# Optimization experiments

Measured on AMD Instinct MI355X. Metric: run time of the kernel, lower is better.

Reference implementation:

```python
import jax, jax.numpy as jnp
import numpy as np
from functools import partial

B, T, H, W = 8, 256, 64, 64
D_MODEL, N_LAYERS, D_STATE = 256, 6, 16
D_INNER = 2 * D_MODEL
DT_RANK = 16  # ceil(256/16)
D_CONV = 4
CNN_Z = 32


def setup_inputs() -> dict:
    key = jax.random.key(0)
    ks = iter(jax.random.split(key, 64))
    r = lambda shape, s=0.02: jax.random.normal(next(ks), shape, dtype=jnp.float32) * s
    inp = {
        'x': jax.random.normal(next(ks), (B, T, 1, H, W), dtype=jnp.float32),
        # frozen CNN spatial encoder (1->16->32->32, stride-2 convs, global avg pool)
        'cnn_w1': r((16, 1, 3, 3)), 'cnn_b1': jnp.zeros((16,)),
        'cnn_w2': r((32, 16, 3, 3)), 'cnn_b2': jnp.zeros((32,)),
        'cnn_w3': r((32, 32, 3, 3)), 'cnn_b3': jnp.zeros((32,)),
        # fc_s2t: 32 -> 256
        'fc_w': r((D_MODEL, CNN_Z)), 'fc_b': jnp.zeros((D_MODEL,)),
        # Mamba, stacked over layers
        'norm_w': jnp.ones((N_LAYERS, D_MODEL)),
        'in_proj_w': r((N_LAYERS, 2 * D_INNER, D_MODEL)),
        'conv1d_w': r((N_LAYERS, D_INNER, D_CONV)),
        'conv1d_b': jnp.zeros((N_LAYERS, D_INNER)),
        'x_proj_w': r((N_LAYERS, DT_RANK + 2 * D_STATE, D_INNER)),
        'dt_proj_w': r((N_LAYERS, D_INNER, DT_RANK)),
        'dt_proj_b': jnp.full((N_LAYERS, D_INNER), -4.6),  # softplus ~ 0.01
        'A_log': jnp.tile(jnp.log(jnp.arange(1, D_STATE + 1, dtype=jnp.float32))[None, None, :], (N_LAYERS, D_INNER, 1)),
        'Dp': jnp.ones((N_LAYERS, D_INNER)),
        'out_proj_w': r((N_LAYERS, D_MODEL, D_INNER)),
        'norm_f_w': jnp.ones((D_MODEL,)),
        # prediction head: 256 -> 64 -> 1
        'head_w1': r((D_MODEL // 4, D_MODEL)), 'head_b1': jnp.zeros((D_MODEL // 4,)),
        'head_w2': r((1, D_MODEL // 4)), 'head_b2': jnp.zeros((1,)),
    }
    return inp


def _conv2d(x, w, b, stride):
    y = jax.lax.conv_general_dilated(x, w, (stride, stride), 'SAME',
                                     dimension_numbers=('NCHW', 'OIHW', 'NCHW'))
    return jax.nn.relu(y + b[None, :, None, None])


def _rmsnorm(x, w, eps=1e-5):
    return x * jax.lax.rsqrt(jnp.mean(x * x, axis=-1, keepdims=True) + eps) * w


def _selective_scan(u, delta, A, Bm, Cm, Dvec):
    # u,delta: (B,L,E); A: (E,N); Bm,Cm: (B,L,N); D: (E,)
    deltaA = jnp.exp(delta[..., None] * A)                       # (B,L,E,N)
    deltaBu = delta[..., None] * Bm[:, :, None, :] * u[..., None]  # (B,L,E,N)

    def step(h, inputs):
        dA, dBu, c = inputs
        h = dA * h + dBu                    # (B,E,N)
        y = jnp.einsum('ben,bn->be', h, c)  # (B,E)
        return h, y

    h0 = jnp.zeros((u.shape[0], u.shape[2], A.shape[1]), u.dtype)
    xs = (deltaA.transpose(1, 0, 2, 3), deltaBu.transpose(1, 0, 2, 3), Cm.transpose(1, 0, 2))
    _, ys = jax.lax.scan(step, h0, xs)
    return ys.transpose(1, 0, 2) + u * Dvec  # (B,L,E)


def _mamba_block(x, nw, ipw, cw, cb, xpw, dpw, dpb, a_log, dvec, opw):
    b, l, d = x.shape
    xz = _rmsnorm(x, nw) @ ipw.T                 # (B,L,2E)
    xin, z = jnp.split(xz, 2, axis=-1)
    # causal depthwise conv1d, kernel 4
    xc = xin.transpose(0, 2, 1)                  # (B,E,L)
    xc = jax.lax.conv_general_dilated(xc, cw[:, None, :], (1,), [(D_CONV - 1, 0)],
                                      feature_group_count=D_INNER,
                                      dimension_numbers=('NCH', 'OIH', 'NCH'))
    xin = jax.nn.silu((xc + cb[None, :, None]).transpose(0, 2, 1))  # (B,L,E)
    dbc = xin @ xpw.T                             # (B,L,dtr+2N)
    dt, Bm, Cm = jnp.split(dbc, [DT_RANK, DT_RANK + D_STATE], axis=-1)
    delta = jax.nn.softplus(dt @ dpw.T + dpb)     # (B,L,E)
    A = -jnp.exp(a_log)                           # (E,N)
    y = _selective_scan(xin, delta, A, Bm, Cm, dvec)
    y = y * jax.nn.silu(z)
    return x + y @ opw.T


def reference(x, cnn_w1, cnn_b1, cnn_w2, cnn_b2, cnn_w3, cnn_b3, fc_w, fc_b,
              norm_w, in_proj_w, conv1d_w, conv1d_b, x_proj_w, dt_proj_w, dt_proj_b,
              A_log, Dp, out_proj_w, norm_f_w, head_w1, head_b1, head_w2, head_b2):
    b, t = x.shape[:2]
    # spatial encoder per frame
    f = x.reshape(b * t, 1, H, W)
    f = _conv2d(f, cnn_w1, cnn_b1, 2)
    f = _conv2d(f, cnn_w2, cnn_b2, 2)
    f = _conv2d(f, cnn_w3, cnn_b3, 2)
    z1 = jnp.mean(f, axis=(2, 3)).reshape(b, t, CNN_Z)   # (B,T,32)
    h = z1 @ fc_w.T + fc_b                                # (B,T,256)
    for i in range(N_LAYERS):
        h = _mamba_block(h, norm_w[i], in_proj_w[i], conv1d_w[i], conv1d_b[i],
                         x_proj_w[i], dt_proj_w[i], dt_proj_b[i], A_log[i], Dp[i], out_proj_w[i])
    z2 = _rmsnorm(h, norm_f_w)
    hh = jax.nn.gelu(z2 @ head_w1.T + head_b1)
    logits = hh @ head_w2.T + head_b2                     # (B,T,1)
    w = jax.nn.softmax(logits, axis=-2)
    w = w.at[:, 0, 0].set(0.0)
    return w
```

## Files before the change

kernel.cpp:

```cpp
#include <hip/hip_runtime.h>
#include <hip/hip_bf16.h>
#include <math.h>

#define Bb 8
#define Tt 256
#define DM 256
#define DI 512
#define NL 6
#define DS 16
#define DTR 16

#define OFF_H     0u
#define OFF_XZ    524288u
#define OFF_DBCP  2621440u
#define OFF_HH    3014656u
#define OFF_LOGIT 3145728u
#define OFF_XNB   3147776u
#define OFF_UB    3278848u
#define OFF_YBF   3540992u
#define OFF_WIP   3803136u
#define OFF_WXP   4589568u
#define OFF_WOP   4663296u

__device__ __forceinline__ float siluf(float x) { return x / (1.f + __expf(-x)); }

typedef __attribute__((ext_vector_type(8))) short bf16x8;
typedef __attribute__((ext_vector_type(4))) short bf16x4;
typedef __attribute__((ext_vector_type(4))) float f32x4;
typedef __attribute__((ext_vector_type(4))) unsigned int u32x4;

__device__ __forceinline__ unsigned short f2bf(float x) {
  unsigned u = __float_as_uint(x);
  u += 0x7FFFu + ((u >> 16) & 1u);
  return (unsigned short)(u >> 16);
}
__device__ __forceinline__ float bf2f(unsigned short u) {
  return __uint_as_float((unsigned)u << 16);
}
__device__ __forceinline__ float ldf(const float* p) { return *p; }
__device__ __forceinline__ float ldf(const unsigned short* p) { return bf2f(*p); }

__global__ __launch_bounds__(256) void cvt_all_kernel(
    const float* __restrict__ s0, unsigned short* __restrict__ d0, int n0,
    const float* __restrict__ s1, unsigned short* __restrict__ d1, int n1,
    const float* __restrict__ s2, unsigned short* __restrict__ d2, int n2) {
  int i = blockIdx.x * 256 + threadIdx.x;
  const float* s; unsigned short* d; int j = i;
  if (j < n0) { s = s0; d = d0; }
  else { j -= n0; if (j < n1) { s = s1; d = d1; }
         else { j -= n1; if (j >= n2) return; s = s2; d = d2; } }
  float4 v = ((const float4*)s)[j];
  bf16x4 o;
  o[0] = (short)f2bf(v.x); o[1] = (short)f2bf(v.y);
  o[2] = (short)f2bf(v.z); o[3] = (short)f2bf(v.w);
  ((bf16x4*)d)[j] = o;
}

__global__ __launch_bounds__(256) void cnn_fc_mfma(
    const float* __restrict__ x,
    const float* __restrict__ w1, const float* __restrict__ b1,
    const float* __restrict__ w2, const float* __restrict__ b2,
    const float* __restrict__ w3, const float* __restrict__ b3,
    const float* __restrict__ fcw, const float* __restrict__ fcb,
    float* __restrict__ hout) {
  __shared__ __align__(16) unsigned short ldsu[31024];
  __shared__ float s_pool[32];
  const int tid = threadIdx.x;
  const int f = blockIdx.x;
  const int lane = tid & 63;
  const int lc = lane & 15;
  const int fq = lane >> 4;
  const int wv = tid >> 6;

  const int FR = 0;
  const int W2 = 0;
  const int C1 = 6400;
  const int C2 = 22800;
  const int W3 = 0;

  {
    const float* xin = x + (size_t)f * 4096;
#pragma unroll
    for (int r = 0; r < 4; ++r) {
      float4 v = ((const float4*)xin)[r * 256 + tid];
      bf16x4 o;
      o[0] = (short)f2bf(v.x); o[1] = (short)f2bf(v.y);
      o[2] = (short)f2bf(v.z); o[3] = (short)f2bf(v.w);
      *(bf16x4*)&ldsu[FR + (r * 256 + tid) * 4] = o;
    }
    if (tid < 8)  ((unsigned*)&ldsu[C1 + 1024 * 16])[tid] = 0u;
    if (tid < 16) ((unsigned*)&ldsu[C2 + 256 * 32])[tid] = 0u;
    if (tid < 32) s_pool[tid] = 0.f;
  }
  __syncthreads();

#pragma unroll
  for (int r = 0; r < 4; ++r) {
    int p = r * 256 + tid;
    int oy = p >> 5, ox = p & 31;
    float in9[9];
#pragma unroll
    for (int ky = 0; ky < 3; ++ky) {
      int iy = 2 * oy + ky;
#pragma unroll
      for (int kx = 0; kx < 3; ++kx) {
        int ix = 2 * ox + kx;
        in9[ky * 3 + kx] = (iy < 64 && ix < 64) ? bf2f(ldsu[FR + iy * 64 + ix]) : 0.f;
      }
    }
    bf16x8 o0, o1;
#pragma unroll
    for (int oc = 0; oc < 8; ++oc) {
      float s = b1[oc];
#pragma unroll
      for (int k = 0; k < 9; ++k) s += w1[oc * 9 + k] * in9[k];
      o0[oc] = (short)f2bf(fmaxf(s, 0.f));
    }
#pragma unroll
    for (int oc = 0; oc < 8; ++oc) {
      float s = b1[8 + oc];
#pragma unroll
      for (int k = 0; k < 9; ++k) s += w1[(8 + oc) * 9 + k] * in9[k];
      o1[oc] = (short)f2bf(fmaxf(s, 0.f));
    }
    *(bf16x8*)&ldsu[C1 + p * 16] = o0;
    *(bf16x8*)&ldsu[C1 + p * 16 + 8] = o1;
  }
  __syncthreads();

  for (int r = 0; r < 20; ++r) {
    int i = r * 256 + tid;
    int kt = i >> 10, rem = i & 1023;
    int oc = rem >> 5, k = rem & 31;
    int tap = 2 * kt + (k >> 4), ic = k & 15;
    float v = (tap < 9) ? w2[oc * 144 + ic * 9 + tap] : 0.f;
    ldsu[W2 + (kt * 32 + oc) * 40 + k] = f2bf(v);
  }
  __syncthreads();

  {
    f32x4 acc[2][4] = {};
    for (int kt = 0; kt < 5; ++kt) {
      bf16x8 a0 = *(const bf16x8*)&ldsu[W2 + (kt * 32 + lc) * 40 + fq * 8];
      bf16x8 a1 = *(const bf16x8*)&ldsu[W2 + (kt * 32 + 16 + lc) * 40 + fq * 8];
      int tap = 2 * kt + (fq >> 1);
      int t9 = (tap < 9) ? tap : 0;
      int ky = (t9 * 11) >> 5;
      int kx = t9 - ky * 3;
      int ix = 2 * lc + kx;
#pragma unroll
      for (int ni = 0; ni < 4; ++ni) {
        int nt = wv * 4 + ni;
        int iy = 2 * nt + ky;
        int ipos = (tap < 9 && iy < 32 && ix < 32) ? iy * 32 + ix : 1024;
        bf16x8 b = *(const bf16x8*)&ldsu[C1 + ipos * 16 + (fq & 1) * 8];
        acc[0][ni] = __builtin_amdgcn_mfma_f32_16x16x32_bf16(a0, b, acc[0][ni], 0, 0, 0);
        acc[1][ni] = __builtin_amdgcn_mfma_f32_16x16x32_bf16(a1, b, acc[1][ni], 0, 0, 0);
      }
    }
#pragma unroll
    for (int mi = 0; mi < 2; ++mi) {
      int oc0 = mi * 16 + fq * 4;
#pragma unroll
      for (int ni = 0; ni < 4; ++ni) {
        int pos = (wv * 4 + ni) * 16 + lc;
        bf16x4 o;
#pragma unroll
        for (int j = 0; j < 4; ++j)
          o[j] = (short)f2bf(fmaxf(acc[mi][ni][j] + b2[oc0 + j], 0.f));
        int g = mi * 4 + fq;
        int gp = ((((g >> 1) ^ ((pos >> 1) & 3)) << 1) | (g & 1));
        *(bf16x4*)&ldsu[C2 + pos * 32 + gp * 4] = o;
      }
    }
  }
  __syncthreads();

  for (int r = 0; r < 36; ++r) {
    int i = r * 256 + tid;
    int tap = i >> 10, rem = i & 1023;
    int oc = rem >> 5, ic = rem & 31;
    ldsu[W3 + (tap * 32 + oc) * 40 + ic] = f2bf(w3[oc * 288 + ic * 9 + tap]);
  }
  __syncthreads();

  {
    const int mh = wv >> 1, nb = wv & 1;
    f32x4 acc[2] = {};
#pragma unroll
    for (int tap = 0; tap < 9; ++tap) {
      const int ky = tap / 3, kx = tap % 3;
      bf16x8 a = *(const bf16x8*)&ldsu[W3 + (tap * 32 + mh * 16 + lc) * 40 + fq * 8];
#pragma unroll
      for (int ni = 0; ni < 2; ++ni) {
        int pos = (nb * 2 + ni) * 16 + lc;
        int py = pos >> 3, px = pos & 7;
        int iy = 2 * py + ky, ix = 2 * px + kx;
        int ipos = (iy < 16 && ix < 16) ? iy * 16 + ix : 256;
        int sp = fq ^ ((ipos >> 1) & 3);
        bf16x8 b = *(const bf16x8*)&ldsu[C2 + ipos * 32 + sp * 8];
        acc[ni] = __builtin_amdgcn_mfma_f32_16x16x32_bf16(a, b, acc[ni], 0, 0, 0);
      }
    }
    int oc0 = mh * 16 + fq * 4;
#pragma unroll
    for (int j = 0; j < 4; ++j) {
      float v = fmaxf(acc[0][j] + b3[oc0 + j], 0.f) +
                fmaxf(acc[1][j] + b3[oc0 + j], 0.f);
      v += __shfl_xor(v, 1);
      v += __shfl_xor(v, 2);
      v += __shfl_xor(v, 4);
      v += __shfl_xor(v, 8);
      if (lc == 0) atomicAdd(&s_pool[oc0 + j], v);
    }
  }
  __syncthreads();

  {
    float dot = 0.f;
#pragma unroll
    for (int k = 0; k < 32; ++k) dot += fcw[tid * 32 + k] * s_pool[k];
    hout[(size_t)f * 256 + tid] = fcb[tid] + dot * (1.f / 64.f);
  }
}

__global__ __launch_bounds__(256) void rmsnorm_kernel(const float* __restrict__ x,
                                                      const float* __restrict__ w,
                                                      unsigned short* __restrict__ ob) {
  __shared__ float red[4];
  int t = blockIdx.x, j = threadIdx.x;
  float v = x[(size_t)t * 256 + j];
  float s = v * v;
#pragma unroll
  for (int m = 32; m; m >>= 1) s += __shfl_xor(s, m);
  if ((j & 63) == 0) red[j >> 6] = s;
  __syncthreads();
  float tot = red[0] + red[1] + red[2] + red[3];
  float r = rsqrtf(tot * (1.f / 256.f) + 1e-5f);
  ob[(size_t)t * 256 + j] = f2bf(v * r * w[j]);
}

__global__ __launch_bounds__(256) void gemm_rn(const float* __restrict__ H,
                                               const float* __restrict__ nw,
                                               const unsigned short* __restrict__ W,
                                               float* __restrict__ C) {
  __shared__ __align__(16) unsigned short sA[64 * 260];
  __shared__ __align__(16) unsigned short sW[64 * 72];
  __shared__ float s_r[64];
  const int tid = threadIdx.x;
  const int m0 = blockIdx.x * 64, n0 = blockIdx.y * 64;
  const int srow = tid >> 2, sseg = tid & 3;
  {
    const float4* gA4 = (const float4*)(H + (size_t)(m0 + srow) * 256 + sseg * 64);
    const float4* nw4 = (const float4*)(nw + sseg * 64);
    float ss = 0.f;
#pragma unroll
    for (int q = 0; q < 16; ++q) {
      float4 v = gA4[q];
      float4 wv = nw4[q];
      ss += v.x * v.x + v.y * v.y + v.z * v.z + v.w * v.w;
      bf16x4 o;
      o[0] = (short)f2bf(v.x * wv.x); o[1] = (short)f2bf(v.y * wv.y);
      o[2] = (short)f2bf(v.z * wv.z); o[3] = (short)f2bf(v.w * wv.w);
      *(bf16x4*)&sA[srow * 260 + sseg * 64 + q * 4] = o;
    }
    ss += __shfl_xor(ss, 1);
    ss += __shfl_xor(ss, 2);
    if ((tid & 3) == 0) s_r[srow] = rsqrtf(ss * (1.f / 256.f) + 1e-5f);
  }
  const unsigned short* gW = W + (size_t)(n0 + srow) * 256 + sseg * 16;
  u32x4 rw0 = ((const u32x4*)gW)[0];
  u32x4 rw1 = ((const u32x4*)gW)[1];
  *(u32x4*)&sW[srow * 72 + sseg * 16] = rw0;
  *(u32x4*)&sW[srow * 72 + sseg * 16 + 8] = rw1;
  __syncthreads();

  const int wv = tid >> 6, wm = wv >> 1, wn = wv & 1;
  const int fr = tid & 15;
  const int fq = (tid >> 4) & 3;
  f32x4 acc[2][2] = {};

  for (int kt = 0; kt < 4; ++kt) {
    if (kt < 3) {
      rw0 = ((const u32x4*)(gW + (kt + 1) * 64))[0];
      rw1 = ((const u32x4*)(gW + (kt + 1) * 64))[1];
    }
#pragma unroll
    for (int ks = 0; ks < 2; ++ks) {
      bf16x8 a0 = *(const bf16x8*)&sA[(wm * 32 + fr) * 260 + kt * 64 + ks * 32 + fq * 8];
      bf16x8 a1 = *(const bf16x8*)&sA[(wm * 32 + 16 + fr) * 260 + kt * 64 + ks * 32 + fq * 8];
      bf16x8 b0 = *(const bf16x8*)&sW[(wn * 32 + fr) * 72 + ks * 32 + fq * 8];
      bf16x8 b1 = *(const bf16x8*)&sW[(wn * 32 + 16 + fr) * 72 + ks * 32 + fq * 8];
      acc[0][0] = __builtin_amdgcn_mfma_f32_16x16x32_bf16(a0, b0, acc[0][0], 0, 0, 0);
      acc[0][1] = __builtin_amdgcn_mfma_f32_16x16x32_bf16(a0, b1, acc[0][1], 0, 0, 0);
      acc[1][0] = __builtin_amdgcn_mfma_f32_16x16x32_bf16(a1, b0, acc[1][0], 0, 0, 0);
      acc[1][1] = __builtin_amdgcn_mfma_f32_16x16x32_bf16(a1, b1, acc[1][1], 0, 0, 0);
    }
    if (kt < 3) {
      __syncthreads();
      *(u32x4*)&sW[srow * 72 + sseg * 16] = rw0;
      *(u32x4*)&sW[srow * 72 + sseg * 16 + 8] = rw1;
      __syncthreads();
    }
  }

#pragma unroll
  for (int mr = 0; mr < 2; ++mr) {
#pragma unroll
    for (int nr = 0; nr < 2; ++nr) {
      int n = n0 + wn * 32 + nr * 16 + fr;
#pragma unroll
      for (int j = 0; j < 4; ++j) {
        int ml = wm * 32 + mr * 16 + fq * 4 + j;
        C[(size_t)(m0 + ml) * 1024 + n] = acc[mr][nr][j] * s_r[ml];
      }
    }
  }
}

__global__ __launch_bounds__(256) void gemm_bb_acc(const unsigned short* __restrict__ A,
                                                   const unsigned short* __restrict__ W,
                                                   float* __restrict__ C,
                                                   int M, int N, int K) {
  __shared__ __align__(16) unsigned short sA[64 * 72];
  __shared__ __align__(16) unsigned short sW[64 * 72];
  const int tid = threadIdx.x;
  const int m0 = blockIdx.x * 64, n0 = blockIdx.y * 64;
  const int ksz = K / (int)gridDim.z;
  const int koff = blockIdx.z * ksz;
  const int srow = tid >> 2, sseg = tid & 3;
  const unsigned short* gA = A + (size_t)(m0 + srow) * K + koff + sseg * 16;
  const unsigned short* gW = W + (size_t)(n0 + srow) * K + koff + sseg * 16;
  const int wv = tid >> 6, wm = wv >> 1, wn = wv & 1;
  const int fr = tid & 15;
  const int fq = (tid >> 4) & 3;
  f32x4 acc[2][2] = {};

  const int NT = ksz >> 6;
  u32x4 ra0, ra1, rw0, rw1;
  ra0 = ((const u32x4*)gA)[0]; ra1 = ((const u32x4*)gA)[1];
  rw0 = ((const u32x4*)gW)[0]; rw1 = ((const u32x4*)gW)[1];
  *(u32x4*)&sA[srow * 72 + sseg * 16] = ra0;
  *(u32x4*)&sA[srow * 72 + sseg * 16 + 8] = ra1;
  *(u32x4*)&sW[srow * 72 + sseg * 16] = rw0;
  *(u32x4*)&sW[srow * 72 + sseg * 16 + 8] = rw1;
  __syncthreads();

  for (int kt = 0; kt < NT; ++kt) {
    if (kt + 1 < NT) {
      ra0 = ((const u32x4*)(gA + (kt + 1) * 64))[0];
      ra1 = ((const u32x4*)(gA + (kt + 1) * 64))[1];
      rw0 = ((const u32x4*)(gW + (kt + 1) * 64))[0];
      rw1 = ((const u32x4*)(gW + (kt + 1) * 64))[1];
    }
#pragma unroll
    for (int ks = 0; ks < 2; ++ks) {
      bf16x8 a0 = *(const bf16x8*)&sA[(wm * 32 + fr) * 72 + ks * 32 + fq * 8];
      bf16x8 a1 = *(const bf16x8*)&sA[(wm * 32 + 16 + fr) * 72 + ks * 32 + fq * 8];
      bf16x8 b0 = *(const bf16x8*)&sW[(wn * 32 + fr) * 72 + ks * 32 + fq * 8];
      bf16x8 b1 = *(const bf16x8*)&sW[(wn * 32 + 16 + fr) * 72 + ks * 32 + fq * 8];
      acc[0][0] = __builtin_amdgcn_mfma_f32_16x16x32_bf16(a0, b0, acc[0][0], 0, 0, 0);
      acc[0][1] = __builtin_amdgcn_mfma_f32_16x16x32_bf16(a0, b1, acc[0][1], 0, 0, 0);
      acc[1][0] = __builtin_amdgcn_mfma_f32_16x16x32_bf16(a1, b0, acc[1][0], 0, 0, 0);
      acc[1][1] = __builtin_amdgcn_mfma_f32_16x16x32_bf16(a1, b1, acc[1][1], 0, 0, 0);
    }
    __syncthreads();
    if (kt + 1 < NT) {
      *(u32x4*)&sA[srow * 72 + sseg * 16] = ra0;
      *(u32x4*)&sA[srow * 72 + sseg * 16 + 8] = ra1;
      *(u32x4*)&sW[srow * 72 + sseg * 16] = rw0;
      *(u32x4*)&sW[srow * 72 + sseg * 16 + 8] = rw1;
      __syncthreads();
    }
  }

#pragma unroll
  for (int mr = 0; mr < 2; ++mr) {
#pragma unroll
    for (int nr = 0; nr < 2; ++nr) {
      int n = n0 + wn * 32 + nr * 16 + fr;
#pragma unroll
      for (int j = 0; j < 4; ++j) {
        int m = m0 + wm * 32 + mr * 16 + fq * 4 + j;
        atomicAdd(&C[(size_t)m * N + n], acc[mr][nr][j]);
      }
    }
  }
}

__global__ __launch_bounds__(256) void gemm_xp(const unsigned short* __restrict__ A,
                                               const unsigned short* __restrict__ W,
                                               float* __restrict__ Cp) {
  __shared__ __align__(16) unsigned short sA[64 * 72];
  __shared__ __align__(16) unsigned short sW[64 * 72];
  const int tid = threadIdx.x;
  const int m0 = blockIdx.x * 64;
  const int koff = blockIdx.y * 128;
  const int srow = tid >> 2, sseg = tid & 3;
  int wrow = (srow < 48) ? srow : 0;
  const unsigned short* gA = A + (size_t)(m0 + srow) * 512 + koff + sseg * 16;
  const unsigned short* gW = W + (size_t)wrow * 512 + koff + sseg * 16;
  const int wv = tid >> 6, wm = wv >> 1, wn = wv & 1;
  const int fr = tid & 15;
  const int fq = (tid >> 4) & 3;
  f32x4 acc[2][2] = {};

  u32x4 ra0, ra1, rw0, rw1;
  ra0 = ((const u32x4*)gA)[0]; ra1 = ((const u32x4*)gA)[1];
  rw0 = ((const u32x4*)gW)[0]; rw1 = ((const u32x4*)gW)[1];
  *(u32x4*)&sA[srow * 72 + sseg * 16] = ra0;
  *(u32x4*)&sA[srow * 72 + sseg * 16 + 8] = ra1;
  *(u32x4*)&sW[srow * 72 + sseg * 16] = rw0;
  *(u32x4*)&sW[srow * 72 + sseg * 16 + 8] = rw1;
  __syncthreads();

  for (int kt = 0; kt < 2; ++kt) {
    if (kt == 0) {
      ra0 = ((const u32x4*)(gA + 64))[0];
      ra1 = ((const u32x4*)(gA + 64))[1];
      rw0 = ((const u32x4*)(gW + 64))[0];
      rw1 = ((const u32x4*)(gW + 64))[1];
    }
#pragma unroll
    for (int ks = 0; ks < 2; ++ks) {
      bf16x8 a0 = *(const bf16x8*)&sA[(wm * 32 + fr) * 72 + ks * 32 + fq * 8];
      bf16x8 a1 = *(const bf16x8*)&sA[(wm * 32 + 16 + fr) * 72 + ks * 32 + fq * 8];
      bf16x8 b0 = *(const bf16x8*)&sW[(wn * 32 + fr) * 72 + ks * 32 + fq * 8];
      bf16x8 b1 = *(const bf16x8*)&sW[(wn * 32 + 16 + fr) * 72 + ks * 32 + fq * 8];
      acc[0][0] = __builtin_amdgcn_mfma_f32_16x16x32_bf16(a0, b0, acc[0][0], 0, 0, 0);
      acc[0][1] = __builtin_amdgcn_mfma_f32_16x16x32_bf16(a0, b1, acc[0][1], 0, 0, 0);
      acc[1][0] = __builtin_amdgcn_mfma_f32_16x16x32_bf16(a1, b0, acc[1][0], 0, 0, 0);
      acc[1][1] = __builtin_amdgcn_mfma_f32_16x16x32_bf16(a1, b1, acc[1][1], 0, 0, 0);
    }
    if (kt == 0) {
      __syncthreads();
      *(u32x4*)&sA[srow * 72 + sseg * 16] = ra0;
      *(u32x4*)&sA[srow * 72 + sseg * 16 + 8] = ra1;
      *(u32x4*)&sW[srow * 72 + sseg * 16] = rw0;
      *(u32x4*)&sW[srow * 72 + sseg * 16 + 8] = rw1;
      __syncthreads();
    }
  }

  float* Co = Cp + (size_t)blockIdx.y * 2048 * 48;
#pragma unroll
  for (int mr = 0; mr < 2; ++mr) {
#pragma unroll
    for (int nr = 0; nr < 2; ++nr) {
      int n = wn * 32 + nr * 16 + fr;
      if (n < 48) {
#pragma unroll
        for (int j = 0; j < 4; ++j) {
          int m = m0 + wm * 32 + mr * 16 + fq * 4 + j;
          Co[(size_t)m * 48 + n] = acc[mr][nr][j];
        }
      }
    }
  }
}

__global__ __launch_bounds__(256) void conv1d_silu_kernel(const float* __restrict__ xz,
                                                          const float* __restrict__ cw,
                                                          const float* __restrict__ cb,
                                                          unsigned short* __restrict__ ub) {
  int idx = blockIdx.x * 256 + threadIdx.x;
  int e = idx & (DI - 1);
  int bt = idx >> 9;
  int t = bt & (Tt - 1);
  int b = bt >> 8;
  float s = cb[e];
#pragma unroll
  for (int j = 0; j < 4; ++j) {
    int tt = t - 3 + j;
    if (tt >= 0) s += cw[e * 4 + j] * xz[((size_t)(b * Tt + tt)) * (2 * DI) + e];
  }
  ub[idx] = f2bf(siluf(s));
}

__global__ __launch_bounds__(1024) void scan_kernel(const float* __restrict__ dbcp,
                                                    const unsigned short* __restrict__ ub,
                                                    const float* __restrict__ xz,
                                                    const float* __restrict__ A_log,
                                                    const float* __restrict__ Dp,
                                                    const float* __restrict__ dpw,
                                                    const float* __restrict__ dpb,
                                                    unsigned short* __restrict__ ybf) {
  __shared__ float sD[256][16];
  __shared__ float sU[256][16];
  __shared__ float sB[256][16];
  __shared__ float sC[256][16];
  __shared__ float sY[256][16];
  __shared__ float s_dpwT[16][17];
  __shared__ float s_dpb[16];
  const int tid = threadIdx.x;
  const int b = blockIdx.x >> 5;
  const int e0 = (blockIdx.x & 31) << 4;
  const int chunk = tid >> 8;
  const int el = (tid >> 4) & 15;
  const int n = tid & 15;
  const int e = e0 + el;
  const float An = -__expf(A_log[e * 16 + n]);
  const float Dv = Dp[e];
  const size_t rowbase = (size_t)b * Tt;

  if (tid < 256) s_dpwT[tid & 15][tid >> 4] = dpw[(size_t)(e0 + (tid >> 4)) * DTR + (tid & 15)];
  if (tid >= 256 && tid < 272) s_dpb[tid - 256] = dpb[e0 + tid - 256];

#pragma unroll
  for (int k = 0; k < 4; ++k) {
    int idx = k * 1024 + tid;
    int row = idx >> 4, col = idx & 15;
    size_t gb = (rowbase + row) * 48;
    float dt = 0.f, Bv = 0.f, Cv = 0.f;
#pragma unroll
    for (int kz = 0; kz < 4; ++kz) {
      const float* p = dbcp + (size_t)kz * 2048 * 48 + gb;
      dt += p[col]; Bv += p[16 + col]; Cv += p[32 + col];
    }
    sY[row][col] = dt;
    sB[row][col] = Bv;
    sC[row][col] = Cv;
    sU[row][col] = bf2f(ub[(rowbase + row) * DI + e0 + col]);
  }
  __syncthreads();

#pragma unroll
  for (int k = 0; k < 4; ++k) {
    int idx = k * 1024 + tid;
    int t = idx >> 4, l = idx & 15;
    float a = s_dpb[l];
#pragma unroll
    for (int kk = 0; kk < 16; ++kk) a += sY[t][kk] * s_dpwT[kk][l];
    sD[t][l] = (a > 20.f) ? a : log1pf(__expf(a));
  }
  __syncthreads();

  float h = 0.f, ap = 1.f;
  const int t0 = chunk * 64;
#pragma unroll 4
  for (int t = t0; t < t0 + 64; ++t) {
    float dv = sD[t][el];
    float dA = __expf(dv * An);
    h = dA * h + dv * sB[t][n] * sU[t][el];
    ap *= dA;
  }
  float* hloc   = &sY[0][0];
  float* aprod  = &sY[64][0];
  float* startH = &sY[128][0];
  const int sidx = el * 16 + n;
  hloc[chunk * 256 + sidx] = h;
  aprod[chunk * 256 + sidx] = ap;
  __syncthreads();

  if (chunk == 0) {
    float H = 0.f;
    startH[sidx] = 0.f;
#pragma unroll
    for (int c = 0; c < 3; ++c) {
      H = aprod[c * 256 + sidx] * H + hloc[c * 256 + sidx];
      startH[(c + 1) * 256 + sidx] = H;
    }
  }
  __syncthreads();
  float h2 = startH[chunk * 256 + sidx];
  __syncthreads();

#pragma unroll 4
  for (int t = t0; t < t0 + 64; ++t) {
    float dv = sD[t][el];
    float uv = sU[t][el];
    float dA = __expf(dv * An);
    h2 = dA * h2 + dv * sB[t][n] * uv;
    float p = h2 * sC[t][n];
    p += __shfl_xor(p, 1);
    p += __shfl_xor(p, 2);
    p += __shfl_xor(p, 4);
    p += __shfl_xor(p, 8);
    if (n == 0) sY[t][el] = p + uv * Dv;
  }
  __syncthreads();

#pragma unroll
  for (int k = 0; k < 4; ++k) {
    int idx = k * 1024 + tid;
    int t = idx >> 4, col = idx & 15;
    float zv = xz[(rowbase + t) * (2 * DI) + DI + e0 + col];
    ybf[(rowbase + t) * DI + e0 + col] = f2bf(sY[t][col] * siluf(zv));
  }
}

template <int ACT, typename AT>
__global__ __launch_bounds__(256) void gemm_nt(const AT* __restrict__ A, int lda,
                                               const float* __restrict__ W,
                                               const float* __restrict__ bias,
                                               float* __restrict__ C,
                                               int M, int N, int K) {
  __shared__ __align__(16) float sA[16][68];
  __shared__ __align__(16) float sW[16][68];
  const int m0 = blockIdx.x * 64;
  const int n0 = blockIdx.y * 64;
  const int tid = threadIdx.x;
  const int lk = tid & 15, lm = tid >> 4;
  const int tx = tid & 15, ty = tid >> 4;
  float acc[4][4] = {};

  for (int k0 = 0; k0 < K; k0 += 16) {
#pragma unroll
    for (int p = 0; p < 4; ++p) {
      int m = p * 16 + lm;
      sA[lk][m] = ldf(&A[(size_t)(m0 + m) * lda + k0 + lk]);
    }
#pragma unroll
    for (int p = 0; p < 4; ++p) {
      int n = p * 16 + lm;
      sW[lk][n] = (n0 + n < N) ? W[(size_t)(n0 + n) * K + k0 + lk] : 0.f;
    }
    __syncthreads();
#pragma unroll
    for (int k = 0; k < 16; ++k) {
      float4 a = *(const float4*)&sA[k][ty * 4];
      float4 b = *(const float4*)&sW[k][tx * 4];
      acc[0][0] += a.x * b.x; acc[0][1] += a.x * b.y; acc[0][2] += a.x * b.z; acc[0][3] += a.x * b.w;
      acc[1][0] += a.y * b.x; acc[1][1] += a.y * b.y; acc[1][2] += a.y * b.z; acc[1][3] += a.y * b.w;
      acc[2][0] += a.z * b.x; acc[2][1] += a.z * b.y; acc[2][2] += a.z * b.z; acc[2][3] += a.z * b.w;
      acc[3][0] += a.w * b.x; acc[3][1] += a.w * b.y; acc[3][2] += a.w * b.z; acc[3][3] += a.w * b.w;
    }
    __syncthreads();
  }
#pragma unroll
  for (int i = 0; i < 4; ++i) {
    int m = m0 + ty * 4 + i;
#pragma unroll
    for (int j = 0; j < 4; ++j) {
      int n = n0 + tx * 4 + j;
      if (n < N) {
        float v = acc[i][j];
        if (ACT == 3) {
          v += bias[n];
          float t3 = v * v * v;
          v = 0.5f * v * (1.f + tanhf(0.7978845608028654f * (v + 0.044715f * t3)));
        }
        C[(size_t)m * N + n] = v;
      }
    }
  }
}

__global__ __launch_bounds__(256) void head_kernel(const float* __restrict__ hh,
                                                   const float* __restrict__ w2,
                                                   const float* __restrict__ b2,
                                                   float* __restrict__ out) {
  __shared__ float redm[4], reds[4];
  int b = blockIdx.x, t = threadIdx.x;
  const float4* row = (const float4*)(hh + ((size_t)b * 256 + t) * 64);
  float v = b2[0];
#pragma unroll
  for (int q = 0; q < 16; ++q) {
    float4 a = row[q];
    float4 w = ((const float4*)w2)[q];
    v += a.x * w.x + a.y * w.y + a.z * w.z + a.w * w.w;
  }
  float m = v;
#pragma unroll
  for (int k = 32; k; k >>= 1) m = fmaxf(m, __shfl_xor(m, k));
  if ((t & 63) == 0) redm[t >> 6] = m;
  __syncthreads();
  m = fmaxf(fmaxf(redm[0], redm[1]), fmaxf(redm[2], redm[3]));
  float e = __expf(v - m);
  float s = e;
#pragma unroll
  for (int k = 32; k; k >>= 1) s += __shfl_xor(s, k);
  if ((t & 63) == 0) reds[t >> 6] = s;
  __syncthreads();
  s = reds[0] + reds[1] + reds[2] + reds[3];
  out[b * 256 + t] = (t == 0) ? 0.f : e / s;
}

extern "C" void kernel_launch(void* const* d_in, const int* in_sizes, int n_in,
                              void* d_out, int out_size, void* d_ws, size_t ws_size,
                              hipStream_t stream) {
  const float* x      = (const float*)d_in[0];
  const float* cnn_w1 = (const float*)d_in[1];
  const float* cnn_b1 = (const float*)d_in[2];
  const float* cnn_w2 = (const float*)d_in[3];
  const float* cnn_b2 = (const float*)d_in[4];
  const float* cnn_w3 = (const float*)d_in[5];
  const float* cnn_b3 = (const float*)d_in[6];
  const float* fc_w   = (const float*)d_in[7];
  const float* fc_b   = (const float*)d_in[8];
  const float* norm_w = (const float*)d_in[9];
  const float* ipw    = (const float*)d_in[10];
  const float* cw     = (const float*)d_in[11];
  const float* cb     = (const float*)d_in[12];
  const float* xpw    = (const float*)d_in[13];
  const float* dpw    = (const float*)d_in[14];
  const float* dpb    = (const float*)d_in[15];
  const float* A_log  = (const float*)d_in[16];
  const float* Dp     = (const float*)d_in[17];
  const float* opw    = (const float*)d_in[18];
  const float* nfw    = (const float*)d_in[19];
  const float* hw1    = (const float*)d_in[20];
  const float* hb1    = (const float*)d_in[21];
  const float* hw2    = (const float*)d_in[22];
  const float* hb2    = (const float*)d_in[23];

  float* ws    = (float*)d_ws;
  float* h     = ws + OFF_H;
  float* xz    = ws + OFF_XZ;
  float* dbcp  = ws + OFF_DBCP;
  float* hh    = ws + OFF_HH;
  float* logit = ws + OFF_LOGIT;  (void)logit;
  unsigned short* xnb = (unsigned short*)(ws + OFF_XNB);
  unsigned short* ub  = (unsigned short*)(ws + OFF_UB);
  unsigned short* ybf = (unsigned short*)(ws + OFF_YBF);
  unsigned short* wip = (unsigned short*)(ws + OFF_WIP);
  unsigned short* wxp = (unsigned short*)(ws + OFF_WXP);
  unsigned short* wop = (unsigned short*)(ws + OFF_WOP);

  const int nv0 = NL * 2 * DI * DM / 4, nv1 = NL * 48 * DI / 4, nv2 = NL * DM * DI / 4;
  cvt_all_kernel<<<(nv0 + nv1 + nv2 + 255) / 256, 256, 0, stream>>>(
      ipw, wip, nv0, xpw, wxp, nv1, opw, wop, nv2);

  cnn_fc_mfma<<<Bb * Tt, 256, 0, stream>>>(x, cnn_w1, cnn_b1, cnn_w2, cnn_b2,
                                           cnn_w3, cnn_b3, fc_w, fc_b, h);

  for (int l = 0; l < NL; ++l) {
    {
      dim3 g(32, 16);
      gemm_rn<<<g, 256, 0, stream>>>(h, norm_w + l * DM,
                                     wip + (size_t)l * 2 * DI * DM, xz);
    }
    conv1d_silu_kernel<<<(Bb * Tt * DI) / 256, 256, 0, stream>>>(
        xz, cw + l * DI * 4, cb + l * DI, ub);
    {
      dim3 g(32, 4);
      gemm_xp<<<g, 256, 0, stream>>>(ub, wxp + (size_t)l * 48 * DI, dbcp);
    }
    scan_kernel<<<Bb * 32, 1024, 0, stream>>>(
        dbcp, ub, xz, A_log + (size_t)l * DI * DS, Dp + l * DI,
        dpw + (size_t)l * DI * DTR, dpb + l * DI, ybf);
    {
      dim3 g(32, 4, 2);
      gemm_bb_acc<<<g, 256, 0, stream>>>(ybf, wop + (size_t)l * DM * DI, h,
                                         Bb * Tt, DM, DI);
    }
  }

  rmsnorm_kernel<<<Bb * Tt, 256, 0, stream>>>(h, nfw, xnb);
  {
    dim3 g(32, 1);
    gemm_nt<3, unsigned short><<<g, 256, 0, stream>>>(xnb, DM, hw1, hb1, hh,
                                                      Bb * Tt, 64, DM);
  }
  head_kernel<<<Bb, 256, 0, stream>>>(hh, hw2, hb2, (float*)d_out);
}
```

Baseline: 589.2 us.

## Fuse conv1d+SiLU into x_proj GEMM and scan; pre-convert CNN weights once

Removes the standalone conv1d_silu kernel and its bf16 ub buffer. The causal depthwise conv and SiLU are now recomputed inside both the x_proj GEMM A-tile load and the scan kernel's u load, reading xz directly. CNN conv2/conv3 weights are converted to bf16 once by a small kernel and read from global memory, instead of being re-transposed into LDS in every one of the 2048 CNN blocks. This saves launches, LDS and syncs, but duplicates the conv computation and its 4x xz reads in two kernels, and the scan now uses fp32 u instead of bf16.

```diff
diff --git a/kernel.cpp b/kernel.cpp
--- a/kernel.cpp
+++ b/kernel.cpp
@@ -16,7 +16,8 @@
 #define OFF_HH    3014656u
 #define OFF_LOGIT 3145728u
 #define OFF_XNB   3147776u
-#define OFF_UB    3278848u
+#define OFF_W2T   3278848u
+#define OFF_W3T   3281408u
 #define OFF_YBF   3540992u
 #define OFF_WIP   3803136u
 #define OFF_WXP   4589568u
@@ -56,14 +57,32 @@
   ((bf16x4*)d)[j] = o;
 }
 
+__global__ __launch_bounds__(256) void cvt_cnnw_kernel(const float* __restrict__ w2,
+                                                       const float* __restrict__ w3,
+                                                       unsigned short* __restrict__ w2t,
+                                                       unsigned short* __restrict__ w3t) {
+  int i = blockIdx.x * 256 + threadIdx.x;
+  if (i < 5120) {
+    int kt = i >> 10, rem = i & 1023;
+    int oc = rem >> 5, k = rem & 31;
+    int tap = 2 * kt + (k >> 4), ic = k & 15;
+    w2t[i] = f2bf((tap < 9) ? w2[oc * 144 + ic * 9 + tap] : 0.f);
+  } else if (i < 5120 + 9216) {
+    int j = i - 5120;
+    int tap = j >> 10, rem = j & 1023;
+    int oc = rem >> 5, ic = rem & 31;
+    w3t[j] = f2bf(w3[oc * 288 + ic * 9 + tap]);
+  }
+}
+
 __global__ __launch_bounds__(256) void cnn_fc_mfma(
     const float* __restrict__ x,
     const float* __restrict__ w1, const float* __restrict__ b1,
-    const float* __restrict__ w2, const float* __restrict__ b2,
-    const float* __restrict__ w3, const float* __restrict__ b3,
+    const unsigned short* __restrict__ w2t, const float* __restrict__ b2,
+    const unsigned short* __restrict__ w3t, const float* __restrict__ b3,
     const float* __restrict__ fcw, const float* __restrict__ fcb,
     float* __restrict__ hout) {
-  __shared__ __align__(16) unsigned short ldsu[31024];
+  __shared__ __align__(16) unsigned short ldsu[24624];
   __shared__ float s_pool[32];
   const int tid = threadIdx.x;
   const int f = blockIdx.x;
@@ -72,11 +91,9 @@
   const int fq = lane >> 4;
   const int wv = tid >> 6;
 
-  const int FR = 0;
-  const int W2 = 0;
-  const int C1 = 6400;
-  const int C2 = 22800;
-  const int W3 = 0;
+  const int C1 = 0;
+  const int C2 = 16400;
+  const int FR = 16400;
 
   {
     const float* xin = x + (size_t)f * 4096;
@@ -128,21 +145,11 @@
   }
   __syncthreads();
 
-  for (int r = 0; r < 20; ++r) {
-    int i = r * 256 + tid;
-    int kt = i >> 10, rem = i & 1023;
-    int oc = rem >> 5, k = rem & 31;
-    int tap = 2 * kt + (k >> 4), ic = k & 15;
-    float v = (tap < 9) ? w2[oc * 144 + ic * 9 + tap] : 0.f;
-    ldsu[W2 + (kt * 32 + oc) * 40 + k] = f2bf(v);
-  }
-  __syncthreads();
-
   {
     f32x4 acc[2][4] = {};
     for (int kt = 0; kt < 5; ++kt) {
-      bf16x8 a0 = *(const bf16x8*)&ldsu[W2 + (kt * 32 + lc) * 40 + fq * 8];
-      bf16x8 a1 = *(const bf16x8*)&ldsu[W2 + (kt * 32 + 16 + lc) * 40 + fq * 8];
+      bf16x8 a0 = *(const bf16x8*)&w2t[(kt * 32 + lc) * 32 + fq * 8];
+      bf16x8 a1 = *(const bf16x8*)&w2t[(kt * 32 + 16 + lc) * 32 + fq * 8];
       int tap = 2 * kt + (fq >> 1);
       int t9 = (tap < 9) ? tap : 0;
       int ky = (t9 * 11) >> 5;
@@ -176,21 +183,13 @@
   }
   __syncthreads();
 
-  for (int r = 0; r < 36; ++r) {
-    int i = r * 256 + tid;
-    int tap = i >> 10, rem = i & 1023;
-    int oc = rem >> 5, ic = rem & 31;
-    ldsu[W3 + (tap * 32 + oc) * 40 + ic] = f2bf(w3[oc * 288 + ic * 9 + tap]);
-  }
-  __syncthreads();
-
   {
     const int mh = wv >> 1, nb = wv & 1;
     f32x4 acc[2] = {};
 #pragma unroll
     for (int tap = 0; tap < 9; ++tap) {
       const int ky = tap / 3, kx = tap % 3;
-      bf16x8 a = *(const bf16x8*)&ldsu[W3 + (tap * 32 + mh * 16 + lc) * 40 + fq * 8];
+      bf16x8 a = *(const bf16x8*)&w3t[(tap * 32 + mh * 16 + lc) * 32 + fq * 8];
 #pragma unroll
       for (int ni = 0; ni < 2; ++ni) {
         int pos = (nb * 2 + ni) * 16 + lc;
@@ -388,7 +387,9 @@
   }
 }
 
-__global__ __launch_bounds__(256) void gemm_xp(const unsigned short* __restrict__ A,
+__global__ __launch_bounds__(256) void gemm_xp(const float* __restrict__ xz,
+                                               const float* __restrict__ cw,
+                                               const float* __restrict__ cb,
                                                const unsigned short* __restrict__ W,
                                                float* __restrict__ Cp) {
   __shared__ __align__(16) unsigned short sA[64 * 72];
@@ -397,30 +398,49 @@
   const int m0 = blockIdx.x * 64;
   const int koff = blockIdx.y * 128;
   const int srow = tid >> 2, sseg = tid & 3;
+  const int m = m0 + srow;
+  const int t = m & (Tt - 1);
   int wrow = (srow < 48) ? srow : 0;
-  const unsigned short* gA = A + (size_t)(m0 + srow) * 512 + koff + sseg * 16;
   const unsigned short* gW = W + (size_t)wrow * 512 + koff + sseg * 16;
   const int wv = tid >> 6, wm = wv >> 1, wn = wv & 1;
   const int fr = tid & 15;
   const int fq = (tid >> 4) & 3;
   f32x4 acc[2][2] = {};
 
-  u32x4 ra0, ra1, rw0, rw1;
-  ra0 = ((const u32x4*)gA)[0]; ra1 = ((const u32x4*)gA)[1];
-  rw0 = ((const u32x4*)gW)[0]; rw1 = ((const u32x4*)gW)[1];
-  *(u32x4*)&sA[srow * 72 + sseg * 16] = ra0;
-  *(u32x4*)&sA[srow * 72 + sseg * 16 + 8] = ra1;
-  *(u32x4*)&sW[srow * 72 + sseg * 16] = rw0;
-  *(u32x4*)&sW[srow * 72 + sseg * 16 + 8] = rw1;
-  __syncthreads();
-
   for (int kt = 0; kt < 2; ++kt) {
-    if (kt == 0) {
-      ra0 = ((const u32x4*)(gA + 64))[0];
-      ra1 = ((const u32x4*)(gA + 64))[1];
-      rw0 = ((const u32x4*)(gW + 64))[0];
-      rw1 = ((const u32x4*)(gW + 64))[1];
-    }
+    if (kt) __syncthreads();
+    {
+      int ebase = koff + kt * 64 + sseg * 16;
+      unsigned short* pa = &sA[srow * 72 + sseg * 16];
+#pragma unroll
+      for (int q = 0; q < 4; ++q) {
+        int e = ebase + q * 4;
+        const float* cwp = cw + e * 4;
+        float s0 = cb[e], s1 = cb[e + 1], s2 = cb[e + 2], s3 = cb[e + 3];
+#pragma unroll
+        for (int j = 0; j < 4; ++j) {
+          int tt = t - 3 + j;
+          if (tt >= 0) {
+            float4 xv = *(const float4*)&xz[(size_t)(m - 3 + j) * 1024 + e];
+            s0 += cwp[0 * 4 + j] * xv.x;
+            s1 += cwp[1 * 4 + j] * xv.y;
+            s2 += cwp[2 * 4 + j] * xv.z;
+            s3 += cwp[3 * 4 + j] * xv.w;
+          }
+        }
+        bf16x4 o;
+        o[0] = (short)f2bf(siluf(s0)); o[1] = (short)f2bf(siluf(s1));
+        o[2] = (short)f2bf(siluf(s2)); o[3] = (short)f2bf(siluf(s3));
+        *(bf16x4*)&pa[q * 4] = o;
+      }
+    }
+    {
+      u32x4 rw0 = ((const u32x4*)(gW + kt * 64))[0];
+      u32x4 rw1 = ((const u32x4*)(gW + kt * 64))[1];
+      *(u32x4*)&sW[srow * 72 + sseg * 16] = rw0;
+      *(u32x4*)&sW[srow * 72 + sseg * 16 + 8] = rw1;
+    }
+    __syncthreads();
 #pragma unroll
     for (int ks = 0; ks < 2; ++ks) {
       bf16x8 a0 = *(const bf16x8*)&sA[(wm * 32 + fr) * 72 + ks * 32 + fq * 8];
@@ -432,14 +452,6 @@
       acc[1][0] = __builtin_amdgcn_mfma_f32_16x16x32_bf16(a1, b0, acc[1][0], 0, 0, 0);
       acc[1][1] = __builtin_amdgcn_mfma_f32_16x16x32_bf16(a1, b1, acc[1][1], 0, 0, 0);
     }
-    if (kt == 0) {
-      __syncthreads();
-      *(u32x4*)&sA[srow * 72 + sseg * 16] = ra0;
-      *(u32x4*)&sA[srow * 72 + sseg * 16 + 8] = ra1;
-      *(u32x4*)&sW[srow * 72 + sseg * 16] = rw0;
-      *(u32x4*)&sW[srow * 72 + sseg * 16 + 8] = rw1;
-      __syncthreads();
-    }
   }
 
   float* Co = Cp + (size_t)blockIdx.y * 2048 * 48;
@@ -451,35 +463,18 @@
       if (n < 48) {
 #pragma unroll
         for (int j = 0; j < 4; ++j) {
-          int m = m0 + wm * 32 + mr * 16 + fq * 4 + j;
-          Co[(size_t)m * 48 + n] = acc[mr][nr][j];
+          int mm = m0 + wm * 32 + mr * 16 + fq * 4 + j;
+          Co[(size_t)mm * 48 + n] = acc[mr][nr][j];
         }
       }
     }
   }
 }
 
-__global__ __launch_bounds__(256) void conv1d_silu_kernel(const float* __restrict__ xz,
-                                                          const float* __restrict__ cw,
-                                                          const float* __restrict__ cb,
-                                                          unsigned short* __restrict__ ub) {
-  int idx = blockIdx.x * 256 + threadIdx.x;
-  int e = idx & (DI - 1);
-  int bt = idx >> 9;
-  int t = bt & (Tt - 1);
-  int b = bt >> 8;
-  float s = cb[e];
-#pragma unroll
-  for (int j = 0; j < 4; ++j) {
-    int tt = t - 3 + j;
-    if (tt >= 0) s += cw[e * 4 + j] * xz[((size_t)(b * Tt + tt)) * (2 * DI) + e];
-  }
-  ub[idx] = f2bf(siluf(s));
-}
-
 __global__ __launch_bounds__(1024) void scan_kernel(const float* __restrict__ dbcp,
-                                                    const unsigned short* __restrict__ ub,
                                                     const float* __restrict__ xz,
+                                                    const float* __restrict__ cw,
+                                                    const float* __restrict__ cb,
                                                     const float* __restrict__ A_log,
                                                     const float* __restrict__ Dp,
                                                     const float* __restrict__ dpw,
@@ -520,7 +515,14 @@
     sY[row][col] = dt;
     sB[row][col] = Bv;
     sC[row][col] = Cv;
-    sU[row][col] = bf2f(ub[(rowbase + row) * DI + e0 + col]);
+    int ec = e0 + col;
+    float uv = cb[ec];
+#pragma unroll
+    for (int j = 0; j < 4; ++j) {
+      int tt = row - 3 + j;
+      if (tt >= 0) uv += cw[ec * 4 + j] * xz[(size_t)(rowbase + tt) * 1024 + ec];
+    }
+    sU[row][col] = siluf(uv);
   }
   __syncthreads();
 
@@ -709,9 +711,9 @@
   float* xz    = ws + OFF_XZ;
   float* dbcp  = ws + OFF_DBCP;
   float* hh    = ws + OFF_HH;
-  float* logit = ws + OFF_LOGIT;  (void)logit;
   unsigned short* xnb = (unsigned short*)(ws + OFF_XNB);
-  unsigned short* ub  = (unsigned short*)(ws + OFF_UB);
+  unsigned short* w2t = (unsigned short*)(ws + OFF_W2T);
+  unsigned short* w3t = (unsigned short*)(ws + OFF_W3T);
   unsigned short* ybf = (unsigned short*)(ws + OFF_YBF);
   unsigned short* wip = (unsigned short*)(ws + OFF_WIP);
   unsigned short* wxp = (unsigned short*)(ws + OFF_WXP);
@@ -720,9 +722,10 @@
   const int nv0 = NL * 2 * DI * DM / 4, nv1 = NL * 48 * DI / 4, nv2 = NL * DM * DI / 4;
   cvt_all_kernel<<<(nv0 + nv1 + nv2 + 255) / 256, 256, 0, stream>>>(
       ipw, wip, nv0, xpw, wxp, nv1, opw, wop, nv2);
-
-  cnn_fc_mfma<<<Bb * Tt, 256, 0, stream>>>(x, cnn_w1, cnn_b1, cnn_w2, cnn_b2,
-                                           cnn_w3, cnn_b3, fc_w, fc_b, h);
+  cvt_cnnw_kernel<<<57, 256, 0, stream>>>(cnn_w2, cnn_w3, w2t, w3t);
+
+  cnn_fc_mfma<<<Bb * Tt, 256, 0, stream>>>(x, cnn_w1, cnn_b1, w2t, cnn_b2,
+                                           w3t, cnn_b3, fc_w, fc_b, h);
 
   for (int l = 0; l < NL; ++l) {
     {
@@ -730,14 +733,14 @@
       gemm_rn<<<g, 256, 0, stream>>>(h, norm_w + l * DM,
                                      wip + (size_t)l * 2 * DI * DM, xz);
     }
-    conv1d_silu_kernel<<<(Bb * Tt * DI) / 256, 256, 0, stream>>>(
-        xz, cw + l * DI * 4, cb + l * DI, ub);
     {
       dim3 g(32, 4);
-      gemm_xp<<<g, 256, 0, stream>>>(ub, wxp + (size_t)l * 48 * DI, dbcp);
+      gemm_xp<<<g, 256, 0, stream>>>(xz, cw + l * DI * 4, cb + l * DI,
+                                     wxp + (size_t)l * 48 * DI, dbcp);
     }
     scan_kernel<<<Bb * 32, 1024, 0, stream>>>(
-        dbcp, ub, xz, A_log + (size_t)l * DI * DS, Dp + l * DI,
+        dbcp, xz, cw + l * DI * 4, cb + l * DI,
+        A_log + (size_t)l * DI * DS, Dp + l * DI,
         dpw + (size_t)l * DI * DTR, dpb + l * DI, ybf);
     {
       dim3 g(32, 4, 2);
```

Measured after the change: 578.4 us. No clear change (-1.8%).
